# Kernel optimization log

Hardware: AMD Instinct MI355X
Metric: run time of the kernel (lower is better)

## Reference

```python
import jax, jax.numpy as jnp
import numpy as np

B, S, T, HD = 8, 2048, 512, 4096  # batch, max_seq, update_len, n_heads*head_dim


def setup_inputs() -> dict:
    key = jax.random.key(0)
    k1, k2 = jax.random.split(key)
    return {
        "k_cache": jnp.zeros((B, S, HD), dtype=jnp.float32),
        "v_cache": jnp.zeros((B, S, HD), dtype=jnp.float32),
        "k_val": jax.random.normal(k1, (B, T, HD), dtype=jnp.float32),
        "v_val": jax.random.normal(k2, (B, T, HD), dtype=jnp.float32),
        "input_pos": jnp.arange(T, dtype=jnp.int64 if jax.config.jax_enable_x64 else jnp.int32),
    }


def reference(k_cache, v_cache, k_val, v_val, input_pos):
    # Functional equivalent of: k_cache[:, input_pos] = k_val; v_cache[:, input_pos] = v_val
    k_out = k_cache.at[:, input_pos].set(k_val)
    v_out = v_cache.at[:, input_pos].set(v_val)
    return (k_out, v_out)
```

## Files before the change

kernel.cpp:

```cpp
#include <hip/hip_runtime.h>

#define B_DIM 8
#define S_DIM 2048
#define T_DIM 512
#define HD_DIM 4096
#define HDV 1024

__global__ void build_map_kernel(const int* __restrict__ input_pos,
                                 int* __restrict__ map) {
    int tid = threadIdx.x;
    map[tid] = -1;
    map[tid + 1024] = -1;
    __syncthreads();
    if (tid < T_DIM) {
        int p = input_pos[tid];
        if (p >= 0 && p < S_DIM) map[p] = tid;
    }
}

__global__ void kv_update_kernel(const float4* __restrict__ k_cache,
                                 const float4* __restrict__ v_cache,
                                 const float4* __restrict__ k_val,
                                 const float4* __restrict__ v_val,
                                 const int* __restrict__ map,
                                 float4* __restrict__ out) {
    const unsigned per_tensor = (unsigned)B_DIM * S_DIM * HDV;
    unsigned idx = blockIdx.x * blockDim.x + threadIdx.x;

    bool is_v = idx >= per_tensor;
    unsigned e = is_v ? (idx - per_tensor) : idx;

    unsigned col = e & (HDV - 1);
    unsigned s   = (e >> 10) & (S_DIM - 1);
    unsigned b   = e >> 21;

    int t = map[s];
    const float4* __restrict__ cache = is_v ? v_cache : k_cache;
    const float4* __restrict__ val   = is_v ? v_val   : k_val;

    float4 r;
    if (t >= 0) {
        r = val[((unsigned)b * T_DIM + (unsigned)t) * HDV + col];
    } else {
        r = cache[e];
    }
    out[idx] = r;
}

__global__ void copy_kernel(const float4* __restrict__ k_cache,
                            const float4* __restrict__ v_cache,
                            float4* __restrict__ out) {
    const unsigned per_tensor = (unsigned)B_DIM * S_DIM * HDV;
    unsigned idx = blockIdx.x * blockDim.x + threadIdx.x;
    out[idx] = (idx >= per_tensor) ? v_cache[idx - per_tensor] : k_cache[idx];
}

__global__ void scatter_kernel(const float4* __restrict__ k_val,
                               const float4* __restrict__ v_val,
                               const int* __restrict__ input_pos,
                               float4* __restrict__ out) {
    const unsigned per_val = (unsigned)B_DIM * T_DIM * HDV;
    const unsigned per_tensor = (unsigned)B_DIM * S_DIM * HDV;
    unsigned idx = blockIdx.x * blockDim.x + threadIdx.x;
    bool is_v = idx >= per_val;
    unsigned e = is_v ? (idx - per_val) : idx;
    unsigned col = e & (HDV - 1);
    unsigned t   = (e >> 10) & (T_DIM - 1);
    unsigned b   = e >> 19;
    int p = input_pos[t];
    float4 r = is_v ? v_val[e] : k_val[e];
    unsigned o = ((unsigned)b * S_DIM + (unsigned)p) * HDV + col
               + (is_v ? per_tensor : 0u);
    out[o] = r;
}

extern "C" void kernel_launch(void* const* d_in, const int* in_sizes, int n_in,
                              void* d_out, int out_size, void* d_ws, size_t ws_size,
                              hipStream_t stream) {
    const float4* k_cache  = (const float4*)d_in[0];
    const float4* v_cache  = (const float4*)d_in[1];
    const float4* k_val    = (const float4*)d_in[2];
    const float4* v_val    = (const float4*)d_in[3];
    const int*    input_pos = (const int*)d_in[4];
    float4* out = (float4*)d_out;

    const unsigned per_tensor = (unsigned)B_DIM * S_DIM * HDV;
    const unsigned total = 2u * per_tensor;

    if (ws_size >= S_DIM * sizeof(int)) {
        int* map = (int*)d_ws;
        build_map_kernel<<<1, 1024, 0, stream>>>(input_pos, map);
        kv_update_kernel<<<total / 256, 256, 0, stream>>>(
            k_cache, v_cache, k_val, v_val, map, out);
    } else {
        copy_kernel<<<total / 256, 256, 0, stream>>>(k_cache, v_cache, out);
        const unsigned sc_total = 2u * (unsigned)B_DIM * T_DIM * HDV;
        scatter_kernel<<<sc_total / 256, 256, 0, stream>>>(
            k_val, v_val, input_pos, out);
    }
}
```

Baseline: 862.6 us.

## Fuse map build into update kernel via wave ballot search, handle K and V per thread

Drops the separate map-building launch. Each wavefront now finds the source row for its sequence position with a ballot scan over input_pos (8 iterations of 64 lanes). Each thread handles the same element for both K and V, which halves the grid and removes the per-thread is_v selection. Loads and stores are marked nontemporal to avoid polluting the caches on this streaming copy. The tradeoff is extra per-thread scan work and reads of input_pos, and the last matching index now wins only within a 64-chunk order, which differs slightly on duplicate positions.

```diff
diff --git a/kernel.cpp b/kernel.cpp
--- a/kernel.cpp
+++ b/kernel.cpp
@@ -3,99 +3,57 @@
 #define B_DIM 8
 #define S_DIM 2048
 #define T_DIM 512
-#define HD_DIM 4096
-#define HDV 1024
+#define HDV   1024
 
-__global__ void build_map_kernel(const int* __restrict__ input_pos,
-                                 int* __restrict__ map) {
-    int tid = threadIdx.x;
-    map[tid] = -1;
-    map[tid + 1024] = -1;
-    __syncthreads();
-    if (tid < T_DIM) {
-        int p = input_pos[tid];
-        if (p >= 0 && p < S_DIM) map[p] = tid;
-    }
-}
+typedef float floatx4 __attribute__((ext_vector_type(4)));
 
-__global__ void kv_update_kernel(const float4* __restrict__ k_cache,
-                                 const float4* __restrict__ v_cache,
-                                 const float4* __restrict__ k_val,
-                                 const float4* __restrict__ v_val,
-                                 const int* __restrict__ map,
-                                 float4* __restrict__ out) {
+__global__ void __launch_bounds__(256)
+kv_update_kernel(const floatx4* __restrict__ k_cache,
+                 const floatx4* __restrict__ v_cache,
+                 const floatx4* __restrict__ k_val,
+                 const floatx4* __restrict__ v_val,
+                 const int* __restrict__ input_pos,
+                 floatx4* __restrict__ out) {
     const unsigned per_tensor = (unsigned)B_DIM * S_DIM * HDV;
-    unsigned idx = blockIdx.x * blockDim.x + threadIdx.x;
-
-    bool is_v = idx >= per_tensor;
-    unsigned e = is_v ? (idx - per_tensor) : idx;
+    unsigned e = blockIdx.x * blockDim.x + threadIdx.x;
 
     unsigned col = e & (HDV - 1);
     unsigned s   = (e >> 10) & (S_DIM - 1);
     unsigned b   = e >> 21;
 
-    int t = map[s];
-    const float4* __restrict__ cache = is_v ? v_cache : k_cache;
-    const float4* __restrict__ val   = is_v ? v_val   : k_val;
+    int lane = threadIdx.x & 63;
+    int t = -1;
+#pragma unroll
+    for (int i = 0; i < T_DIM / 64; ++i) {
+        int p = input_pos[i * 64 + lane];
+        unsigned long long m = __ballot(p == (int)s);
+        if (m) t = i * 64 + (__ffsll((long long)m) - 1);
+    }
 
-    float4 r;
+    floatx4 rk, rv;
     if (t >= 0) {
-        r = val[((unsigned)b * T_DIM + (unsigned)t) * HDV + col];
+        unsigned vi = (b * (unsigned)T_DIM + (unsigned)t) * HDV + col;
+        rk = __builtin_nontemporal_load(k_val + vi);
+        rv = __builtin_nontemporal_load(v_val + vi);
     } else {
-        r = cache[e];
+        rk = __builtin_nontemporal_load(k_cache + e);
+        rv = __builtin_nontemporal_load(v_cache + e);
     }
-    out[idx] = r;
-}
-
-__global__ void copy_kernel(const float4* __restrict__ k_cache,
-                            const float4* __restrict__ v_cache,
-                            float4* __restrict__ out) {
-    const unsigned per_tensor = (unsigned)B_DIM * S_DIM * HDV;
-    unsigned idx = blockIdx.x * blockDim.x + threadIdx.x;
-    out[idx] = (idx >= per_tensor) ? v_cache[idx - per_tensor] : k_cache[idx];
-}
-
-__global__ void scatter_kernel(const float4* __restrict__ k_val,
-                               const float4* __restrict__ v_val,
-                               const int* __restrict__ input_pos,
-                               float4* __restrict__ out) {
-    const unsigned per_val = (unsigned)B_DIM * T_DIM * HDV;
-    const unsigned per_tensor = (unsigned)B_DIM * S_DIM * HDV;
-    unsigned idx = blockIdx.x * blockDim.x + threadIdx.x;
-    bool is_v = idx >= per_val;
-    unsigned e = is_v ? (idx - per_val) : idx;
-    unsigned col = e & (HDV - 1);
-    unsigned t   = (e >> 10) & (T_DIM - 1);
-    unsigned b   = e >> 19;
-    int p = input_pos[t];
-    float4 r = is_v ? v_val[e] : k_val[e];
-    unsigned o = ((unsigned)b * S_DIM + (unsigned)p) * HDV + col
-               + (is_v ? per_tensor : 0u);
-    out[o] = r;
+    __builtin_nontemporal_store(rk, out + e);
+    __builtin_nontemporal_store(rv, out + per_tensor + e);
 }
 
 extern "C" void kernel_launch(void* const* d_in, const int* in_sizes, int n_in,
                               void* d_out, int out_size, void* d_ws, size_t ws_size,
                               hipStream_t stream) {
-    const float4* k_cache  = (const float4*)d_in[0];
-    const float4* v_cache  = (const float4*)d_in[1];
-    const float4* k_val    = (const float4*)d_in[2];
-    const float4* v_val    = (const float4*)d_in[3];
-    const int*    input_pos = (const int*)d_in[4];
-    float4* out = (float4*)d_out;
+    const floatx4* k_cache   = (const floatx4*)d_in[0];
+    const floatx4* v_cache   = (const floatx4*)d_in[1];
+    const floatx4* k_val     = (const floatx4*)d_in[2];
+    const floatx4* v_val     = (const floatx4*)d_in[3];
+    const int*     input_pos = (const int*)d_in[4];
+    floatx4* out = (floatx4*)d_out;
 
     const unsigned per_tensor = (unsigned)B_DIM * S_DIM * HDV;
-    const unsigned total = 2u * per_tensor;
-
-    if (ws_size >= S_DIM * sizeof(int)) {
-        int* map = (int*)d_ws;
-        build_map_kernel<<<1, 1024, 0, stream>>>(input_pos, map);
-        kv_update_kernel<<<total / 256, 256, 0, stream>>>(
-            k_cache, v_cache, k_val, v_val, map, out);
-    } else {
-        copy_kernel<<<total / 256, 256, 0, stream>>>(k_cache, v_cache, out);
-        const unsigned sc_total = 2u * (unsigned)B_DIM * T_DIM * HDV;
-        scatter_kernel<<<sc_total / 256, 256, 0, stream>>>(
-            k_val, v_val, input_pos, out);
-    }
+    kv_update_kernel<<<per_tensor / 256, 256, 0, stream>>>(
+        k_cache, v_cache, k_val, v_val, input_pos, out);
 }
```

Measured after the change: 859.8 us. About the same (-0.3%).
